# Kernel tuning notes

Hardware: AMD Instinct MI355X
Metric: run time of the kernel (lower is better)

Reference implementation:

```python
import jax, jax.numpy as jnp
import numpy as np

B, R, C, H, W = 4, 2, 19, 256, 512


def setup_inputs() -> dict:
    key = jax.random.key(0)
    k1, k2, k3 = jax.random.split(key, 3)
    return {
        "ref_pred": jax.random.normal(k1, (B, R, C, H, W), dtype=jnp.float32),
        # motion vectors in quarter-pel units (divided by 4 inside forward);
        # scale so displacements span a few pixels
        "ref_mv": jax.random.normal(k2, (B, R, 2, H, W), dtype=jnp.float32) * 8.0,
        "ref_weight": jax.random.uniform(k3, (B, R, 1, H, W), dtype=jnp.float32),
    }


def _warp(img, mv):
    """Bilinear backward warp (grid_sample, zeros padding).
    img: [N, C, H, W], mv: [N, 2, H, W] pixel displacements (x, y)."""
    N, Ch, Hh, Ww = img.shape
    ys, xs = jnp.meshgrid(jnp.arange(Hh, dtype=mv.dtype),
                          jnp.arange(Ww, dtype=mv.dtype), indexing="ij")
    gx = xs + mv[:, 0]  # [N, H, W] sample x-coordinate
    gy = ys + mv[:, 1]  # [N, H, W] sample y-coordinate
    x0 = jnp.floor(gx); y0 = jnp.floor(gy)
    x1 = x0 + 1.0;      y1 = y0 + 1.0
    wx1 = gx - x0; wx0 = 1.0 - wx1
    wy1 = gy - y0; wy0 = 1.0 - wy1

    img_flat = img.reshape(N, Ch, Hh * Ww)

    def samp(iy, ix):
        valid = ((ix >= 0) & (ix <= Ww - 1) & (iy >= 0) & (iy <= Hh - 1))
        iyc = jnp.clip(iy, 0, Hh - 1).astype(jnp.int32)
        ixc = jnp.clip(ix, 0, Ww - 1).astype(jnp.int32)
        lin = (iyc * Ww + ixc).reshape(N, 1, Hh * Ww)
        vals = jnp.take_along_axis(
            img_flat, jnp.broadcast_to(lin, (N, Ch, Hh * Ww)), axis=2
        ).reshape(N, Ch, Hh, Ww)
        return vals * valid.astype(img.dtype)[:, None]

    out = (samp(y0, x0) * (wy0 * wx0)[:, None]
           + samp(y0, x1) * (wy0 * wx1)[:, None]
           + samp(y1, x0) * (wy1 * wx0)[:, None]
           + samp(y1, x1) * (wy1 * wx1)[:, None])
    return out


def reference(ref_pred, ref_mv, ref_weight):
    Bb, Rr = ref_pred.shape[:2]
    pred = ref_pred.reshape(Bb * Rr, *ref_pred.shape[2:])   # [B*R, C, H, W]
    mv = ref_mv.reshape(Bb * Rr, *ref_mv.shape[2:]) / 4.0    # quarter-pel -> pixel
    # eval mode, eval_noise_sigma=0 -> no noise added
    warped = _warp(pred, mv)                                  # [B*R, C, H, W]
    w = ref_weight.reshape(Bb * Rr, *ref_weight.shape[2:])   # [B*R, 1, H, W]
    warped = warped * w
    return warped.reshape(Bb, Rr, *warped.shape[1:]).sum(axis=1)  # [B, C, H, W]
```

## Files before the change

kernel.cpp:

```cpp
#include <hip/hip_runtime.h>

constexpr int B = 4, R = 2, C = 19, H = 256, W = 512;
constexpr int HW = H * W;

constexpr int BX = 64, BY = 16;
constexpr int NBX = W / BX;
constexpr int NBY = H / BY;
constexpr int NSPAT = B * NBX * NBY;
constexpr int NCHUNK = 4;

constexpr int TW = 88;
constexpr int TH = 37;
constexpr int TILE_N = TW * TH;
constexpr int TILE_V4 = TILE_N / 4;

#define GLD_LDS16(gsrc, ldst)                                                  \
    __builtin_amdgcn_global_load_lds(                                          \
        (const __attribute__((address_space(1))) void*)(gsrc),                 \
        (__attribute__((address_space(3))) void*)(ldst), 16, 0, 0)

__global__ __launch_bounds__(256, 4) void mc_warp_kernel(
    const float* __restrict__ pred,
    const float* __restrict__ mv,
    const float* __restrict__ wgt,
    float* __restrict__ out)
{
    __shared__ float tiles[2][2][TILE_N];

    int t = threadIdx.x;
    int xcd  = blockIdx.x & 7;
    int slot = blockIdx.x >> 3;
    int vblk = xcd * (NSPAT / 8) + slot;
    int bx   = vblk & (NBX - 1);
    int by   = (vblk >> 3) & (NBY - 1);
    int b    = vblk >> 7;
    int x0 = bx * BX, y0 = by * BY;
    int lane = t & 63, wv = t >> 6;
    int x  = x0 + lane;
    int yb = y0 + wv * 4;

    int rowbase = min(max(y0 - 10, 0), H - TH);
    int colbase = min(max(x0 - 12, 0), W - TW);

    const float* pl0 = pred + (size_t)(b * R + 0) * C * HW;
    const float* pl1 = pred + (size_t)(b * R + 1) * C * HW;
    const float* st0 = pl0 + (size_t)rowbase * W + colbase;
    const float* st1 = pl1 + (size_t)rowbase * W + colbase;

    int cbeg = (C * blockIdx.y) / NCHUNK;
    int cend = (C * (blockIdx.y + 1)) / NCHUNK;

    {
        const float* s0 = st0 + (size_t)cbeg * HW;
        const float* s1 = st1 + (size_t)cbeg * HW;
        #pragma unroll
        for (int i = 0; i < 4; ++i) {
            int idx = t + i * 256;
            if (idx < TILE_V4) {
                int row = idx / 22;
                int off = idx * 4 + row * (W - TW);
                GLD_LDS16(s0 + off, &tiles[0][0][idx * 4]);
                GLD_LDS16(s1 + off, &tiles[0][1][idx * 4]);
            }
        }
    }

    int   off0[R][4], off1[R][4];
    int   offL0[R][4], offL1[R][4], offG0[R][4], offG1[R][4];
    float wq[R][4][4];
    int flag = 0;

    #pragma unroll
    for (int r = 0; r < R; ++r) {
        const float* mvx = mv + (size_t)((b * R + r) * 2) * HW;
        const float* mvy = mvx + HW;
        const float* wp  = wgt + (size_t)(b * R + r) * HW;
        #pragma unroll
        for (int p = 0; p < 4; ++p) {
            int yy = yb + p;
            size_t ro = (size_t)yy * W + x;
            float mx = mvx[ro], my = mvy[ro], wr = wp[ro];

            float gx = (float)x  + mx * 0.25f;
            float gy = (float)yy + my * 0.25f;
            float fx0 = floorf(gx), fy0 = floorf(gy);
            float wx1 = gx - fx0, wx0 = 1.0f - wx1;
            float wy1 = gy - fy0, wy0 = 1.0f - wy1;
            int ix0 = (int)fx0, iy0 = (int)fy0;
            int ix1 = ix0 + 1,  iy1 = iy0 + 1;

            int base = min(max(ix0, 0), W - 2);
            float wA = (ix0 == base)     ? wx0 : ((ix1 == base)     ? wx1 : 0.0f);
            float wB = (ix1 == base + 1) ? wx1 : ((ix0 == base + 1) ? wx0 : 0.0f);
            float wy0v = ((iy0 >= 0) && (iy0 < H)) ? wy0 * wr : 0.0f;
            float wy1v = ((iy1 >= 0) && (iy1 < H)) ? wy1 * wr : 0.0f;
            int cy0 = min(max(iy0, 0), H - 1);
            int cy1 = min(max(iy1, 0), H - 1);

            int l0 = base - colbase;
            int r0 = cy0 - rowbase, r1 = cy1 - rowbase;
            bool anyx = (wA != 0.0f) || (wB != 0.0f);
            bool anyy = (wy0v != 0.0f) || (wy1v != 0.0f);
            bool cb  = (l0 < 0 || l0 > TW - 2) && anyx && anyy;
            bool rb0 = (r0 < 0 || r0 > TH - 1) && (wy0v != 0.0f) && anyx;
            bool rb1 = (r1 < 0 || r1 > TH - 1) && (wy1v != 0.0f) && anyx;
            flag |= (int)(cb || rb0 || rb1);
            l0 = min(max(l0, 0), TW - 2);
            r0 = min(max(r0, 0), TH - 1);
            r1 = min(max(r1, 0), TH - 1);

            offL0[r][p] = r0 * TW + l0;
            offL1[r][p] = r1 * TW + l0;
            offG0[r][p] = cy0 * W + base;
            offG1[r][p] = cy1 * W + base;
            wq[r][p][0] = wy0v * wA;
            wq[r][p][1] = wy0v * wB;
            wq[r][p][2] = wy1v * wA;
            wq[r][p][3] = wy1v * wB;
        }
    }

    int fbB = __syncthreads_or(flag);
    #pragma unroll
    for (int r = 0; r < R; ++r)
        #pragma unroll
        for (int p = 0; p < 4; ++p) {
            off0[r][p] = fbB ? offG0[r][p] : offL0[r][p];
            off1[r][p] = fbB ? offG1[r][p] : offL1[r][p];
        }

    float* ob = out + (size_t)b * C * HW + (size_t)yb * W + x;

    int cur = 0;
    for (int c = cbeg; c < cend; ++c, cur ^= 1) {
        __syncthreads();

        if (!fbB && c + 1 < cend) {
            const float* s0 = st0 + (size_t)(c + 1) * HW;
            const float* s1 = st1 + (size_t)(c + 1) * HW;
            #pragma unroll
            for (int i = 0; i < 4; ++i) {
                int idx = t + i * 256;
                if (idx < TILE_V4) {
                    int row = idx / 22;
                    int off = idx * 4 + row * (W - TW);
                    GLD_LDS16(s0 + off, &tiles[cur ^ 1][0][idx * 4]);
                    GLD_LDS16(s1 + off, &tiles[cur ^ 1][1][idx * 4]);
                }
            }
        }

        float res[4];
        if (!fbB) {
            const float* tb0 = &tiles[cur][0][0];
            const float* tb1 = &tiles[cur][1][0];
            #pragma unroll
            for (int p = 0; p < 4; ++p) {
                float a00 = tb0[off0[0][p]], a01 = tb0[off0[0][p] + 1];
                float a10 = tb0[off1[0][p]], a11 = tb0[off1[0][p] + 1];
                float b00 = tb1[off0[1][p]], b01 = tb1[off0[1][p] + 1];
                float b10 = tb1[off1[1][p]], b11 = tb1[off1[1][p] + 1];
                res[p] = wq[0][p][0] * a00 + wq[0][p][1] * a01
                       + wq[0][p][2] * a10 + wq[0][p][3] * a11
                       + wq[1][p][0] * b00 + wq[1][p][1] * b01
                       + wq[1][p][2] * b10 + wq[1][p][3] * b11;
            }
        } else {
            const float* pc0 = pl0 + (size_t)c * HW;
            const float* pc1 = pl1 + (size_t)c * HW;
            #pragma unroll
            for (int p = 0; p < 4; ++p) {
                float a00 = pc0[off0[0][p]], a01 = pc0[off0[0][p] + 1];
                float a10 = pc0[off1[0][p]], a11 = pc0[off1[0][p] + 1];
                float b00 = pc1[off0[1][p]], b01 = pc1[off0[1][p] + 1];
                float b10 = pc1[off1[1][p]], b11 = pc1[off1[1][p] + 1];
                res[p] = wq[0][p][0] * a00 + wq[0][p][1] * a01
                       + wq[0][p][2] * a10 + wq[0][p][3] * a11
                       + wq[1][p][0] * b00 + wq[1][p][1] * b01
                       + wq[1][p][2] * b10 + wq[1][p][3] * b11;
            }
        }
        float* oc = ob + (size_t)c * HW;
        #pragma unroll
        for (int p = 0; p < 4; ++p)
            oc[(size_t)p * W] = res[p];
    }
}

extern "C" void kernel_launch(void* const* d_in, const int* in_sizes, int n_in,
                              void* d_out, int out_size, void* d_ws, size_t ws_size,
                              hipStream_t stream) {
    const float* pred = (const float*)d_in[0];
    const float* mv   = (const float*)d_in[1];
    const float* wgt  = (const float*)d_in[2];
    float* out = (float*)d_out;

    dim3 grid(NSPAT, NCHUNK);
    mc_warp_kernel<<<grid, dim3(256), 0, stream>>>(pred, mv, wgt, out);
}
```

Before: 151.9 us.

## Drop LDS tile staging and gather bilinear taps directly from global memory

Removes the double-buffered shared-memory tile path (async global-to-LDS loads, per-channel barriers, and the out-of-tile fallback flag) and always reads the four bilinear taps for both references straight from global memory through the caches. This cuts LDS usage, barrier stalls and the redundant halo loads of each tile. In exchange every tap becomes a scattered global load that depends on L1/L2 hit rates instead of fast LDS reads.

```diff
diff --git a/kernel.cpp b/kernel.cpp
--- a/kernel.cpp
+++ b/kernel.cpp
@@ -9,24 +9,12 @@
 constexpr int NSPAT = B * NBX * NBY;
 constexpr int NCHUNK = 4;
 
-constexpr int TW = 88;
-constexpr int TH = 37;
-constexpr int TILE_N = TW * TH;
-constexpr int TILE_V4 = TILE_N / 4;
-
-#define GLD_LDS16(gsrc, ldst)                                                  \
-    __builtin_amdgcn_global_load_lds(                                          \
-        (const __attribute__((address_space(1))) void*)(gsrc),                 \
-        (__attribute__((address_space(3))) void*)(ldst), 16, 0, 0)
-
 __global__ __launch_bounds__(256, 4) void mc_warp_kernel(
     const float* __restrict__ pred,
     const float* __restrict__ mv,
     const float* __restrict__ wgt,
     float* __restrict__ out)
 {
-    __shared__ float tiles[2][2][TILE_N];
-
     int t = threadIdx.x;
     int xcd  = blockIdx.x & 7;
     int slot = blockIdx.x >> 3;
@@ -39,36 +27,14 @@
     int x  = x0 + lane;
     int yb = y0 + wv * 4;
 
-    int rowbase = min(max(y0 - 10, 0), H - TH);
-    int colbase = min(max(x0 - 12, 0), W - TW);
-
     const float* pl0 = pred + (size_t)(b * R + 0) * C * HW;
     const float* pl1 = pred + (size_t)(b * R + 1) * C * HW;
-    const float* st0 = pl0 + (size_t)rowbase * W + colbase;
-    const float* st1 = pl1 + (size_t)rowbase * W + colbase;
 
     int cbeg = (C * blockIdx.y) / NCHUNK;
     int cend = (C * (blockIdx.y + 1)) / NCHUNK;
 
-    {
-        const float* s0 = st0 + (size_t)cbeg * HW;
-        const float* s1 = st1 + (size_t)cbeg * HW;
-        #pragma unroll
-        for (int i = 0; i < 4; ++i) {
-            int idx = t + i * 256;
-            if (idx < TILE_V4) {
-                int row = idx / 22;
-                int off = idx * 4 + row * (W - TW);
-                GLD_LDS16(s0 + off, &tiles[0][0][idx * 4]);
-                GLD_LDS16(s1 + off, &tiles[0][1][idx * 4]);
-            }
-        }
-    }
-
     int   off0[R][4], off1[R][4];
-    int   offL0[R][4], offL1[R][4], offG0[R][4], offG1[R][4];
     float wq[R][4][4];
-    int flag = 0;
 
     #pragma unroll
     for (int r = 0; r < R; ++r) {
@@ -97,22 +63,8 @@
             int cy0 = min(max(iy0, 0), H - 1);
             int cy1 = min(max(iy1, 0), H - 1);
 
-            int l0 = base - colbase;
-            int r0 = cy0 - rowbase, r1 = cy1 - rowbase;
-            bool anyx = (wA != 0.0f) || (wB != 0.0f);
-            bool anyy = (wy0v != 0.0f) || (wy1v != 0.0f);
-            bool cb  = (l0 < 0 || l0 > TW - 2) && anyx && anyy;
-            bool rb0 = (r0 < 0 || r0 > TH - 1) && (wy0v != 0.0f) && anyx;
-            bool rb1 = (r1 < 0 || r1 > TH - 1) && (wy1v != 0.0f) && anyx;
-            flag |= (int)(cb || rb0 || rb1);
-            l0 = min(max(l0, 0), TW - 2);
-            r0 = min(max(r0, 0), TH - 1);
-            r1 = min(max(r1, 0), TH - 1);
-
-            offL0[r][p] = r0 * TW + l0;
-            offL1[r][p] = r1 * TW + l0;
-            offG0[r][p] = cy0 * W + base;
-            offG1[r][p] = cy1 * W + base;
+            off0[r][p] = cy0 * W + base;
+            off1[r][p] = cy1 * W + base;
             wq[r][p][0] = wy0v * wA;
             wq[r][p][1] = wy0v * wB;
             wq[r][p][2] = wy1v * wA;
@@ -120,65 +72,22 @@
         }
     }
 
-    int fbB = __syncthreads_or(flag);
-    #pragma unroll
-    for (int r = 0; r < R; ++r)
+    float* ob = out + (size_t)b * C * HW + (size_t)yb * W + x;
+
+    for (int c = cbeg; c < cend; ++c) {
+        const float* pc0 = pl0 + (size_t)c * HW;
+        const float* pc1 = pl1 + (size_t)c * HW;
+        float res[4];
         #pragma unroll
         for (int p = 0; p < 4; ++p) {
-            off0[r][p] = fbB ? offG0[r][p] : offL0[r][p];
-            off1[r][p] = fbB ? offG1[r][p] : offL1[r][p];
-        }
-
-    float* ob = out + (size_t)b * C * HW + (size_t)yb * W + x;
-
-    int cur = 0;
-    for (int c = cbeg; c < cend; ++c, cur ^= 1) {
-        __syncthreads();
-
-        if (!fbB && c + 1 < cend) {
-            const float* s0 = st0 + (size_t)(c + 1) * HW;
-            const float* s1 = st1 + (size_t)(c + 1) * HW;
-            #pragma unroll
-            for (int i = 0; i < 4; ++i) {
-                int idx = t + i * 256;
-                if (idx < TILE_V4) {
-                    int row = idx / 22;
-                    int off = idx * 4 + row * (W - TW);
-                    GLD_LDS16(s0 + off, &tiles[cur ^ 1][0][idx * 4]);
-                    GLD_LDS16(s1 + off, &tiles[cur ^ 1][1][idx * 4]);
-                }
-            }
-        }
-
-        float res[4];
-        if (!fbB) {
-            const float* tb0 = &tiles[cur][0][0];
-            const float* tb1 = &tiles[cur][1][0];
-            #pragma unroll
-            for (int p = 0; p < 4; ++p) {
-                float a00 = tb0[off0[0][p]], a01 = tb0[off0[0][p] + 1];
-                float a10 = tb0[off1[0][p]], a11 = tb0[off1[0][p] + 1];
-                float b00 = tb1[off0[1][p]], b01 = tb1[off0[1][p] + 1];
-                float b10 = tb1[off1[1][p]], b11 = tb1[off1[1][p] + 1];
-                res[p] = wq[0][p][0] * a00 + wq[0][p][1] * a01
-                       + wq[0][p][2] * a10 + wq[0][p][3] * a11
-                       + wq[1][p][0] * b00 + wq[1][p][1] * b01
-                       + wq[1][p][2] * b10 + wq[1][p][3] * b11;
-            }
-        } else {
-            const float* pc0 = pl0 + (size_t)c * HW;
-            const float* pc1 = pl1 + (size_t)c * HW;
-            #pragma unroll
-            for (int p = 0; p < 4; ++p) {
-                float a00 = pc0[off0[0][p]], a01 = pc0[off0[0][p] + 1];
-                float a10 = pc0[off1[0][p]], a11 = pc0[off1[0][p] + 1];
-                float b00 = pc1[off0[1][p]], b01 = pc1[off0[1][p] + 1];
-                float b10 = pc1[off1[1][p]], b11 = pc1[off1[1][p] + 1];
-                res[p] = wq[0][p][0] * a00 + wq[0][p][1] * a01
-                       + wq[0][p][2] * a10 + wq[0][p][3] * a11
-                       + wq[1][p][0] * b00 + wq[1][p][1] * b01
-                       + wq[1][p][2] * b10 + wq[1][p][3] * b11;
-            }
+            float a00 = pc0[off0[0][p]], a01 = pc0[off0[0][p] + 1];
+            float a10 = pc0[off1[0][p]], a11 = pc0[off1[0][p] + 1];
+            float b00 = pc1[off0[1][p]], b01 = pc1[off0[1][p] + 1];
+            float b10 = pc1[off1[1][p]], b11 = pc1[off1[1][p] + 1];
+            res[p] = wq[0][p][0] * a00 + wq[0][p][1] * a01
+                   + wq[0][p][2] * a10 + wq[0][p][3] * a11
+                   + wq[1][p][0] * b00 + wq[1][p][1] * b01
+                   + wq[1][p][2] * b10 + wq[1][p][3] * b11;
         }
         float* oc = ob + (size_t)c * HW;
         #pragma unroll
```

New measurement: 202.0 us. 1.33x slower.
